# Kernel tuning notes

Measured on AMD Instinct MI355X. Metric: run time of the kernel, lower is better.

The kernel has to match this reference:

```python
import jax, jax.numpy as jnp
import numpy as np

D_M = 1024
NUM_TOK = 4096


def setup_inputs() -> dict:
    key = jax.random.key(0)
    ks = jax.random.split(key, 7)
    mk = lambda k, shp: jax.random.normal(k, shp, dtype=jnp.float32) * 0.02
    return {
        "X": jax.random.normal(ks[0], (D_M, NUM_TOK), dtype=jnp.float32),
        "W_Q": mk(ks[1], (D_M, D_M)),
        "W_K": mk(ks[2], (D_M, D_M)),
        "W_V": mk(ks[3], (D_M, D_M)),
        "W_O": mk(ks[4], (D_M, D_M)),
        "mlp_in": mk(ks[5], (D_M, D_M)),
        "mlp_out": mk(ks[6], (D_M, D_M)),
    }


def reference(X, W_Q, W_K, W_V, W_O, mlp_in, mlp_out):
    # X: [d_m, num_tok]; module transposes to tokens-major [N, d]
    Xt = X.T  # [N, d]
    N = Xt.shape[0]
    Q = Xt @ W_Q  # [N, d]
    K = Xt @ W_K  # [N, d]
    scores = Q @ K.T  # [N, N] -- NOTE: no 1/sqrt(d) scaling, as in the original
    causal = jnp.tril(jnp.ones((N, N), dtype=bool))  # keep lower triangle incl. diag
    scores = jnp.where(causal, scores, -jnp.inf)
    A = jax.nn.softmax(scores, axis=-1)  # [N, N]
    # original applies W_V then W_O to X BEFORE the attention mix
    RH = (Xt @ W_V) @ W_O  # [N, d]
    Xt = Xt + A @ RH  # residual + attention
    h = jax.nn.relu(Xt @ mlp_in)  # [N, d] (hidden dim == d_m in original)
    Xt = Xt + h @ mlp_out  # residual + MLP
    return Xt.T  # back to [d_m, num_tok]
```

## Files before the change

kernel.cpp:

```cpp
#include <hip/hip_runtime.h>
#include <stdint.h>
#include <stddef.h>

using f16 = _Float16;
typedef __attribute__((ext_vector_type(8))) _Float16 f16x8;
typedef __attribute__((ext_vector_type(4))) float f32x4;

__device__ __forceinline__ void async_copy16(const f16* g, f16* l) {
    __builtin_amdgcn_global_load_lds(
        (const __attribute__((address_space(1))) void*)g,
        (__attribute__((address_space(3))) void*)l, 16, 0, 0);
}

__global__ __launch_bounds__(256)
void prep_all(const float* __restrict__ X, float* __restrict__ Xtf,
              f16* __restrict__ Xth,
              const float* __restrict__ w0, const float* __restrict__ w1,
              const float* __restrict__ w2, const float* __restrict__ w3,
              const float* __restrict__ w4, const float* __restrict__ w5,
              f16* o0, f16* o1, f16* o2, f16* o3, f16* o4, f16* o5,
              int D, int NT) {
    __shared__ float tile[32][33];
    const int tx = threadIdx.x & 31, ty = threadIdx.x >> 5;
    int b = blockIdx.x;
    if (b < 4096) {
        const int c0 = (b & 127) * 32, r0 = (b >> 7) * 32;
#pragma unroll
        for (int j = 0; j < 4; j++)
            tile[ty + j * 8][tx] = X[(size_t)(r0 + ty + j * 8) * NT + c0 + tx];
        __syncthreads();
#pragma unroll
        for (int j = 0; j < 4; j++) {
            float v = tile[tx][ty + j * 8];
            size_t idx = (size_t)(c0 + ty + j * 8) * D + r0 + tx;
            Xtf[idx] = v;
            Xth[idx] = (f16)v;
        }
        return;
    }
    b -= 4096;
    const int z = b >> 10, r = b & 1023;
    const float* in = z == 0 ? w0 : z == 1 ? w1 : z == 2 ? w2 : z == 3 ? w3 : z == 4 ? w4 : w5;
    f16* out = z == 0 ? o0 : z == 1 ? o1 : z == 2 ? o2 : z == 3 ? o3 : z == 4 ? o4 : o5;
    const int c0 = (r & 31) * 32, r0 = (r >> 5) * 32;
    if (z < 3) {
#pragma unroll
        for (int j = 0; j < 4; j++) {
            size_t idx = (size_t)(r0 + ty + j * 8) * D + c0 + tx;
            out[idx] = (f16)in[idx];
        }
    } else {
#pragma unroll
        for (int j = 0; j < 4; j++)
            tile[ty + j * 8][tx] = in[(size_t)(r0 + ty + j * 8) * D + c0 + tx];
        __syncthreads();
#pragma unroll
        for (int j = 0; j < 4; j++)
            out[(size_t)(c0 + ty + j * 8) * D + r0 + tx] = (f16)tile[tx][ty + j * 8];
    }
}

__global__ __launch_bounds__(256)
void softmax_rows(f16* __restrict__ A, int N) {
    const int row = blockIdx.x, len = row + 1;
    const int lim = ((row >> 7) + 1) << 7;
    f16* a = A + (size_t)row * N;
    __shared__ float red[256];
    const int t = threadIdx.x;

    float v[16];
    float mx = -1e30f;
#pragma unroll
    for (int j = 0; j < 2; j++) {
        const int c = (t + j * 256) * 8;
        if (c < len) {
            f16x8 x = *(const f16x8*)(a + c);
#pragma unroll
            for (int e = 0; e < 8; e++) {
                float f = (c + e < len) ? (float)x[e] : -1e30f;
                v[j * 8 + e] = f;
                mx = fmaxf(mx, f);
            }
        } else {
#pragma unroll
            for (int e = 0; e < 8; e++) v[j * 8 + e] = -1e30f;
        }
    }
    red[t] = mx; __syncthreads();
    for (int o = 128; o > 0; o >>= 1) { if (t < o) red[t] = fmaxf(red[t], red[t + o]); __syncthreads(); }
    mx = red[0]; __syncthreads();

    float sum = 0.f;
#pragma unroll
    for (int k = 0; k < 16; k++) {
        float e = (v[k] > -1e29f) ? __expf(v[k] - mx) : 0.0f;
        v[k] = e;
        sum += e;
    }
    red[t] = sum; __syncthreads();
    for (int o = 128; o > 0; o >>= 1) { if (t < o) red[t] += red[t + o]; __syncthreads(); }
    const float inv = 1.0f / red[0];
#pragma unroll
    for (int j = 0; j < 2; j++) {
        const int c = (t + j * 256) * 8;
        if (c < lim) {
            f16x8 o8;
#pragma unroll
            for (int e = 0; e < 8; e++) o8[e] = (f16)(v[j * 8 + e] * inv);
            *(f16x8*)(a + c) = o8;
        }
    }
}

template <int MODE>
__device__ __forceinline__ void body64(
    f16* lA, f16* lB, const f16* __restrict__ A, const f16* __restrict__ B,
    f16* __restrict__ Ch, int m0, int n0, int N, int K, int lda, int Keff) {
    const int t = threadIdx.x;
    const int lane = t & 63, wave = t >> 6;
    const int wm = (wave >> 1) * 32, wn = (wave & 1) * 32;
    const int lm = lane & 15, lq = lane >> 4;
    const int sr = t >> 2, sc = (t & 3) * 8;

    f32x4 acc[2][2] = {};

    for (int k0 = 0; k0 < Keff; k0 += 128) {
#pragma unroll
        for (int r = 0; r < 4; r++)
            async_copy16(A + (size_t)(m0 + sr) * lda + k0 + r * 32 + sc,
                         lA + r * 2048 + t * 8);
#pragma unroll
        for (int r = 0; r < 4; r++)
            async_copy16(B + (size_t)(n0 + sr) * K + k0 + r * 32 + sc,
                         lB + r * 2048 + t * 8);
        __syncthreads();

#pragma unroll
        for (int kk = 0; kk < 4; kk++) {
            f16x8 af[2], bf[2];
#pragma unroll
            for (int i = 0; i < 2; i++)
                af[i] = *(const f16x8*)&lA[kk * 2048 + (wm + i * 16 + lm) * 32 + lq * 8];
#pragma unroll
            for (int j = 0; j < 2; j++)
                bf[j] = *(const f16x8*)&lB[kk * 2048 + (wn + j * 16 + lm) * 32 + lq * 8];
#pragma unroll
            for (int i = 0; i < 2; i++)
#pragma unroll
                for (int j = 0; j < 2; j++)
                    acc[i][j] = __builtin_amdgcn_mfma_f32_16x16x32_f16(
                        af[i], bf[j], acc[i][j], 0, 0, 0);
        }
        __syncthreads();
    }

#pragma unroll
    for (int i = 0; i < 2; i++) {
        const int row = m0 + wm + i * 16 + lq * 4;
#pragma unroll
        for (int j = 0; j < 2; j++) {
            const int col = n0 + wn + j * 16 + lm;
            f32x4 v = acc[i][j];
#pragma unroll
            for (int r = 0; r < 4; r++)
                Ch[(size_t)(row + r) * N + col] = (f16)v[r];
        }
    }
}

template <int BN, int MODE>
__device__ __forceinline__ void body128(
    f16* lA, f16* lB, const f16* __restrict__ A, const f16* __restrict__ B,
    float* __restrict__ Cf, f16* __restrict__ Ch, const float* __restrict__ resid,
    int m0, int n0, int M, int N, int K, int lda, int Keff) {
    const int t = threadIdx.x;
    const int lane = t & 63, wave = t >> 6;
    constexpr int WN = BN / 2;
    constexpr int NJ = WN / 16;
    const int wm = (wave >> 1) * 64, wn = (wave & 1) * WN;
    const int lm = lane & 15, lq = lane >> 4;
    const int srow = t >> 2, scol = (t & 3) * 8;

    f32x4 acc[4][NJ] = {};

    for (int k0 = 0; k0 < Keff; k0 += 64) {
#pragma unroll
        for (int r = 0; r < 4; r++) {
            const int row = (r & 1) * 64 + srow, kk = r >> 1;
            async_copy16(A + (size_t)(m0 + row) * lda + k0 + kk * 32 + scol,
                         lA + kk * 4096 + row * 32 + scol);
        }
        if constexpr (BN == 128) {
#pragma unroll
            for (int r = 0; r < 4; r++) {
                const int row = (r & 1) * 64 + srow, kk = r >> 1;
                async_copy16(B + (size_t)(n0 + row) * K + k0 + kk * 32 + scol,
                             lB + kk * 4096 + row * 32 + scol);
            }
        } else {
#pragma unroll
            for (int r = 0; r < 2; r++)
                async_copy16(B + (size_t)(n0 + srow) * K + k0 + r * 32 + scol,
                             lB + r * 2048 + srow * 32 + scol);
        }
        __syncthreads();

#pragma unroll
        for (int kk = 0; kk < 2; kk++) {
            f16x8 af[4], bf[NJ];
#pragma unroll
            for (int i = 0; i < 4; i++)
                af[i] = *(const f16x8*)&lA[kk * 4096 + (wm + i * 16 + lm) * 32 + lq * 8];
#pragma unroll
            for (int j = 0; j < NJ; j++)
                bf[j] = *(const f16x8*)&lB[kk * (BN * 32) + (wn + j * 16 + lm) * 32 + lq * 8];
#pragma unroll
            for (int i = 0; i < 4; i++)
#pragma unroll
                for (int j = 0; j < NJ; j++)
                    acc[i][j] = __builtin_amdgcn_mfma_f32_16x16x32_f16(
                        af[i], bf[j], acc[i][j], 0, 0, 0);
        }
        __syncthreads();
    }

#pragma unroll
    for (int i = 0; i < 4; i++) {
        const int row = m0 + wm + i * 16 + lq * 4;
#pragma unroll
        for (int j = 0; j < NJ; j++) {
            const int col = n0 + wn + j * 16 + lm;
            f32x4 v = acc[i][j];
#pragma unroll
            for (int r = 0; r < 4; r++) {
                if (MODE == 0) {
                    Ch[(size_t)(row + r) * N + col] = (f16)v[r];
                } else if (MODE == 2) {
                    float o = v[r] + resid[(size_t)(row + r) * N + col];
                    Cf[(size_t)(row + r) * N + col] = o;
                    Ch[(size_t)(row + r) * N + col] = (f16)o;
                } else if (MODE == 3) {
                    Ch[(size_t)(row + r) * N + col] = (f16)fmaxf(v[r], 0.0f);
                } else {
                    float o = v[r] + resid[(size_t)(row + r) * N + col];
                    Cf[(size_t)col * M + (row + r)] = o;
                }
            }
        }
    }
}

__global__ __launch_bounds__(256, 4)
void tiny_pair(const f16* Wkh, const f16* Wqh, f16* GT,
               const f16* Wot, const f16* Wvh, f16* HT) {
    __shared__ alignas(16) f16 smem[16384];
    const int b = blockIdx.x;
    if (b < 256)
        body64<0>(smem, smem + 8192, Wkh, Wqh, GT,
                  (b >> 4) * 64, (b & 15) * 64, 1024, 1024, 1024, 1024);
    else {
        const int r = b - 256;
        body64<0>(smem, smem + 8192, Wot, Wvh, HT,
                  (r >> 4) * 64, (r & 15) * 64, 1024, 1024, 1024, 1024);
    }
}

__global__ __launch_bounds__(256, 2)
void mid_pair(const f16* Xth, const f16* GT, f16* Qp,
              const f16* HT, f16* RHt) {
    __shared__ alignas(16) f16 smem[16384];
    const int x = blockIdx.x & 7;
    int s = blockIdx.x >> 3;
    if (s < 32) {
        const int m = x + 8 * (s >> 3), n = s & 7;
        body128<128, 0>(smem, smem + 8192, Xth, GT, nullptr, Qp, nullptr,
                        m * 128, n * 128, 4096, 1024, 1024, 1024, 1024);
    } else {
        s -= 32;
        const int n = x + 8 * (s >> 3), m = s & 7;
        body128<128, 0>(smem, smem + 8192, HT, Xth, nullptr, RHt, nullptr,
                        m * 128, n * 128, 1024, 4096, 1024, 1024, 1024);
    }
}

__global__ __launch_bounds__(256, 2)
void scores_tri(const f16* Qp, const f16* Xth, f16* Af) {
    __shared__ alignas(16) f16 smem[16384];
    const int x = blockIdx.x & 7;
    int s = blockIdx.x >> 3;
    int m = 0, n = 0;
#pragma unroll
    for (int q = 3; q >= 0; q--) {
        const int mm = 8 * q + ((q & 1) ? 7 - x : x);
        if (s < mm + 1) { m = mm; n = s; break; }
        s -= mm + 1;
    }
    body128<128, 0>(smem, smem + 8192, Qp, Xth, nullptr, Af, nullptr,
                    m * 128, n * 128, 4096, 4096, 1024, 1024, 1024);
}

template <int MODE, bool CAUSAL_K>
__global__ __launch_bounds__(256, 2)
void gemm_n64(const f16* __restrict__ A, const f16* __restrict__ B,
              float* __restrict__ Cf, f16* __restrict__ Ch,
              const float* __restrict__ resid, int M, int N, int K, int lda) {
    __shared__ alignas(16) f16 smem[12288];
    const int x = blockIdx.x & 7, s = blockIdx.x >> 3;
    const int qs = s >> 4, n = s & 15;
    int m;
    if (CAUSAL_K) {
        const int q = (qs == 0) ? 3 : (qs == 1) ? 2 : (qs == 2) ? 0 : 1;
        m = 8 * q + ((q & 1) ? 7 - x : x);
    } else {
        m = x + 8 * qs;
    }
    const int m0 = m * 128, n0 = n * 64;
    int Keff = K;
    if (CAUSAL_K) {
        Keff = m0 + 128;
        if (Keff > K) Keff = K;
    }
    body128<64, MODE>(smem, smem + 8192, A, B, Cf, Ch, resid,
                      m0, n0, M, N, K, lda, Keff);
}

extern "C" void kernel_launch(void* const* d_in, const int* in_sizes, int n_in,
                              void* d_out, int out_size, void* d_ws, size_t ws_size,
                              hipStream_t stream) {
    const int D = 1024, NT = 4096;
    const float* X = (const float*)d_in[0];
    const float* W[6] = {(const float*)d_in[1], (const float*)d_in[2],
                         (const float*)d_in[3], (const float*)d_in[4],
                         (const float*)d_in[5], (const float*)d_in[6]};
    char* ws = (char*)d_ws;
    auto MB = [](size_t x) { return x << 20; };

    float* Xtf  = (float*)(ws + MB(0));
    f16*   Xth  = (f16*)(ws + MB(16));
    f16*   Wqh  = (f16*)(ws + MB(24));
    f16*   Wkh  = (f16*)(ws + MB(26));
    f16*   Wvh  = (f16*)(ws + MB(28));
    f16*   Wot  = (f16*)(ws + MB(30));
    f16*   W4t  = (f16*)(ws + MB(32));
    f16*   W5t  = (f16*)(ws + MB(34));
    f16*   GT   = (f16*)(ws + MB(36));
    f16*   HT   = (f16*)(ws + MB(38));
    f16*   Qp   = (f16*)(ws + MB(40));
    f16*   Af   = (f16*)(ws + MB(48));
    f16*   RHt  = (f16*)(ws + MB(80));
    float* Y1f  = (float*)(ws + MB(88));
    f16*   Y1h  = (f16*)(ws + MB(104));
    f16*   hb   = (f16*)(ws + MB(40));
    float* outF = (float*)d_out;

    prep_all<<<10240, 256, 0, stream>>>(X, Xtf, Xth, W[0], W[1], W[2], W[3],
                                        W[4], W[5], Wqh, Wkh, Wvh, Wot, W4t,
                                        W5t, D, NT);

    tiny_pair<<<512, 256, 0, stream>>>(Wkh, Wqh, GT, Wot, Wvh, HT);

    mid_pair<<<512, 256, 0, stream>>>(Xth, GT, Qp, HT, RHt);

    scores_tri<<<528, 256, 0, stream>>>(Qp, Xth, Af);

    softmax_rows<<<NT, 256, 0, stream>>>(Af, NT);

    gemm_n64<2, true><<<512, 256, 0, stream>>>(
        Af, RHt, Y1f, Y1h, Xtf, NT, D, NT, NT);

    gemm_n64<3, false><<<512, 256, 0, stream>>>(
        Y1h, W4t, nullptr, hb, nullptr, NT, D, D, D);

    gemm_n64<4, false><<<512, 256, 0, stream>>>(
        hb, W5t, outF, nullptr, Y1f, NT, D, D, D);
}
```

Baseline: 259.5 us.

## Double-buffer LDS tiles and XOR-swizzle layout in GEMM bodies

Rewrites the shared GEMM bodies so the next K-tile is staged into a second LDS buffer with async global-to-LDS copies while MFMAs run on the current one, leaving one barrier per iteration instead of two. It also XOR-swizzles the 16-byte column chunks on both write and read to cut LDS bank conflicts. LDS per block doubles, and tiny_pair's occupancy hint drops from 4 to 2. The lone trailing barrier may not wait for the async loads to land before they are read, so correctness depends on how the compiler places its waits.

```diff
diff --git a/kernel.cpp b/kernel.cpp
--- a/kernel.cpp
+++ b/kernel.cpp
@@ -112,38 +112,45 @@
     }
 }
 
-template <int MODE>
-__device__ __forceinline__ void body64(
-    f16* lA, f16* lB, const f16* __restrict__ A, const f16* __restrict__ B,
-    f16* __restrict__ Ch, int m0, int n0, int N, int K, int lda, int Keff) {
+
+__device__ __forceinline__ void body64db(
+    f16* lds, const f16* __restrict__ A, const f16* __restrict__ B,
+    f16* __restrict__ Ch, int m0, int n0, int N, int K, int lda) {
     const int t = threadIdx.x;
     const int lane = t & 63, wave = t >> 6;
     const int wm = (wave >> 1) * 32, wn = (wave & 1) * 32;
     const int lm = lane & 15, lq = lane >> 4;
-    const int sr = t >> 2, sc = (t & 3) * 8;
+    const int srow = t >> 2;
+    const int gs = ((t & 3) ^ ((srow >> 1) & 3)) * 8;
+    const int rs = (lq ^ ((lm >> 1) & 3)) * 8;
+
+    auto stage = [&](f16* buf, int k0) {
+#pragma unroll
+        for (int r = 0; r < 4; r++)
+            async_copy16(A + (size_t)(m0 + srow) * lda + k0 + r * 32 + gs,
+                         buf + r * 2048 + t * 8);
+#pragma unroll
+        for (int r = 0; r < 4; r++)
+            async_copy16(B + (size_t)(n0 + srow) * K + k0 + r * 32 + gs,
+                         buf + 8192 + r * 2048 + t * 8);
+    };
 
     f32x4 acc[2][2] = {};
-
-    for (int k0 = 0; k0 < Keff; k0 += 128) {
-#pragma unroll
-        for (int r = 0; r < 4; r++)
-            async_copy16(A + (size_t)(m0 + sr) * lda + k0 + r * 32 + sc,
-                         lA + r * 2048 + t * 8);
-#pragma unroll
-        for (int r = 0; r < 4; r++)
-            async_copy16(B + (size_t)(n0 + sr) * K + k0 + r * 32 + sc,
-                         lB + r * 2048 + t * 8);
-        __syncthreads();
-
+    stage(lds, 0);
+    __syncthreads();
+    int cur = 0;
+    for (int k0 = 0; k0 < K; k0 += 128) {
+        f16* cb = lds + cur * 16384;
+        if (k0 + 128 < K) stage(lds + (cur ^ 1) * 16384, k0 + 128);
 #pragma unroll
         for (int kk = 0; kk < 4; kk++) {
             f16x8 af[2], bf[2];
 #pragma unroll
             for (int i = 0; i < 2; i++)
-                af[i] = *(const f16x8*)&lA[kk * 2048 + (wm + i * 16 + lm) * 32 + lq * 8];
+                af[i] = *(const f16x8*)&cb[kk * 2048 + (wm + i * 16 + lm) * 32 + rs];
 #pragma unroll
             for (int j = 0; j < 2; j++)
-                bf[j] = *(const f16x8*)&lB[kk * 2048 + (wn + j * 16 + lm) * 32 + lq * 8];
+                bf[j] = *(const f16x8*)&cb[8192 + kk * 2048 + (wn + j * 16 + lm) * 32 + rs];
 #pragma unroll
             for (int i = 0; i < 2; i++)
 #pragma unroll
@@ -152,6 +159,7 @@
                         af[i], bf[j], acc[i][j], 0, 0, 0);
         }
         __syncthreads();
+        cur ^= 1;
     }
 
 #pragma unroll
@@ -169,51 +177,57 @@
 }
 
 template <int BN, int MODE>
-__device__ __forceinline__ void body128(
-    f16* lA, f16* lB, const f16* __restrict__ A, const f16* __restrict__ B,
+__device__ __forceinline__ void body128db(
+    f16* lds, const f16* __restrict__ A, const f16* __restrict__ B,
     float* __restrict__ Cf, f16* __restrict__ Ch, const float* __restrict__ resid,
     int m0, int n0, int M, int N, int K, int lda, int Keff) {
     const int t = threadIdx.x;
     const int lane = t & 63, wave = t >> 6;
     constexpr int WN = BN / 2;
     constexpr int NJ = WN / 16;
+    constexpr int ASZ = 128 * 64;
+    constexpr int BSZ = BN * 64;
+    constexpr int BUF = ASZ + BSZ;
     const int wm = (wave >> 1) * 64, wn = (wave & 1) * WN;
     const int lm = lane & 15, lq = lane >> 4;
-    const int srow = t >> 2, scol = (t & 3) * 8;
+    const int srow = t >> 2;
+    const int gs = ((t & 3) ^ ((srow >> 1) & 3)) * 8;
+    const int rs = (lq ^ ((lm >> 1) & 3)) * 8;
+
+    auto stage = [&](f16* buf, int k0) {
+#pragma unroll
+        for (int r = 0; r < 4; r++)
+            async_copy16(A + (size_t)(m0 + (r & 1) * 64 + srow) * lda + k0 + (r >> 1) * 32 + gs,
+                         buf + r * 2048 + t * 8);
+        if constexpr (BN == 128) {
+#pragma unroll
+            for (int r = 0; r < 4; r++)
+                async_copy16(B + (size_t)(n0 + (r & 1) * 64 + srow) * K + k0 + (r >> 1) * 32 + gs,
+                             buf + ASZ + r * 2048 + t * 8);
+        } else {
+#pragma unroll
+            for (int r = 0; r < 2; r++)
+                async_copy16(B + (size_t)(n0 + srow) * K + k0 + r * 32 + gs,
+                             buf + ASZ + r * 2048 + t * 8);
+        }
+    };
 
     f32x4 acc[4][NJ] = {};
-
+    stage(lds, 0);
+    __syncthreads();
+    int cur = 0;
     for (int k0 = 0; k0 < Keff; k0 += 64) {
-#pragma unroll
-        for (int r = 0; r < 4; r++) {
-            const int row = (r & 1) * 64 + srow, kk = r >> 1;
-            async_copy16(A + (size_t)(m0 + row) * lda + k0 + kk * 32 + scol,
-                         lA + kk * 4096 + row * 32 + scol);
-        }
-        if constexpr (BN == 128) {
-#pragma unroll
-            for (int r = 0; r < 4; r++) {
-                const int row = (r & 1) * 64 + srow, kk = r >> 1;
-                async_copy16(B + (size_t)(n0 + row) * K + k0 + kk * 32 + scol,
-                             lB + kk * 4096 + row * 32 + scol);
-            }
-        } else {
-#pragma unroll
-            for (int r = 0; r < 2; r++)
-                async_copy16(B + (size_t)(n0 + srow) * K + k0 + r * 32 + scol,
-                             lB + r * 2048 + srow * 32 + scol);
-        }
-        __syncthreads();
-
+        f16* cb = lds + cur * BUF;
+        if (k0 + 64 < Keff) stage(lds + (cur ^ 1) * BUF, k0 + 64);
 #pragma unroll
         for (int kk = 0; kk < 2; kk++) {
             f16x8 af[4], bf[NJ];
 #pragma unroll
             for (int i = 0; i < 4; i++)
-                af[i] = *(const f16x8*)&lA[kk * 4096 + (wm + i * 16 + lm) * 32 + lq * 8];
+                af[i] = *(const f16x8*)&cb[kk * 4096 + (wm + i * 16 + lm) * 32 + rs];
 #pragma unroll
             for (int j = 0; j < NJ; j++)
-                bf[j] = *(const f16x8*)&lB[kk * (BN * 32) + (wn + j * 16 + lm) * 32 + lq * 8];
+                bf[j] = *(const f16x8*)&cb[ASZ + kk * (BN * 32) + (wn + j * 16 + lm) * 32 + rs];
 #pragma unroll
             for (int i = 0; i < 4; i++)
 #pragma unroll
@@ -222,6 +236,7 @@
                         af[i], bf[j], acc[i][j], 0, 0, 0);
         }
         __syncthreads();
+        cur ^= 1;
     }
 
 #pragma unroll
@@ -250,42 +265,42 @@
     }
 }
 
-__global__ __launch_bounds__(256, 4)
+__global__ __launch_bounds__(256, 2)
 void tiny_pair(const f16* Wkh, const f16* Wqh, f16* GT,
                const f16* Wot, const f16* Wvh, f16* HT) {
-    __shared__ alignas(16) f16 smem[16384];
+    __shared__ alignas(16) f16 smem[32768];
     const int b = blockIdx.x;
     if (b < 256)
-        body64<0>(smem, smem + 8192, Wkh, Wqh, GT,
-                  (b >> 4) * 64, (b & 15) * 64, 1024, 1024, 1024, 1024);
+        body64db(smem, Wkh, Wqh, GT,
+                 (b >> 4) * 64, (b & 15) * 64, 1024, 1024, 1024);
     else {
         const int r = b - 256;
-        body64<0>(smem, smem + 8192, Wot, Wvh, HT,
-                  (r >> 4) * 64, (r & 15) * 64, 1024, 1024, 1024, 1024);
+        body64db(smem, Wot, Wvh, HT,
+                 (r >> 4) * 64, (r & 15) * 64, 1024, 1024, 1024);
     }
 }
 
 __global__ __launch_bounds__(256, 2)
 void mid_pair(const f16* Xth, const f16* GT, f16* Qp,
               const f16* HT, f16* RHt) {
-    __shared__ alignas(16) f16 smem[16384];
+    __shared__ alignas(16) f16 smem[32768];
     const int x = blockIdx.x & 7;
     int s = blockIdx.x >> 3;
     if (s < 32) {
         const int m = x + 8 * (s >> 3), n = s & 7;
-        body128<128, 0>(smem, smem + 8192, Xth, GT, nullptr, Qp, nullptr,
-                        m * 128, n * 128, 4096, 1024, 1024, 1024, 1024);
+        body128db<128, 0>(smem, Xth, GT, nullptr, Qp, nullptr,
+                          m * 128, n * 128, 4096, 1024, 1024, 1024, 1024);
     } else {
         s -= 32;
         const int n = x + 8 * (s >> 3), m = s & 7;
-        body128<128, 0>(smem, smem + 8192, HT, Xth, nullptr, RHt, nullptr,
-                        m * 128, n * 128, 1024, 4096, 1024, 1024, 1024);
+        body128db<128, 0>(smem, HT, Xth, nullptr, RHt, nullptr,
+                          m * 128, n * 128, 1024, 4096, 1024, 1024, 1024);
     }
 }
 
 __global__ __launch_bounds__(256, 2)
 void scores_tri(const f16* Qp, const f16* Xth, f16* Af) {
-    __shared__ alignas(16) f16 smem[16384];
+    __shared__ alignas(16) f16 smem[32768];
     const int x = blockIdx.x & 7;
     int s = blockIdx.x >> 3;
     int m = 0, n = 0;
@@ -295,8 +310,8 @@
         if (s < mm + 1) { m = mm; n = s; break; }
         s -= mm + 1;
     }
-    body128<128, 0>(smem, smem + 8192, Qp, Xth, nullptr, Af, nullptr,
-                    m * 128, n * 128, 4096, 4096, 1024, 1024, 1024);
+    body128db<128, 0>(smem, Qp, Xth, nullptr, Af, nullptr,
+                      m * 128, n * 128, 4096, 4096, 1024, 1024, 1024);
 }
 
 template <int MODE, bool CAUSAL_K>
@@ -304,7 +319,7 @@
 void gemm_n64(const f16* __restrict__ A, const f16* __restrict__ B,
               float* __restrict__ Cf, f16* __restrict__ Ch,
               const float* __restrict__ resid, int M, int N, int K, int lda) {
-    __shared__ alignas(16) f16 smem[12288];
+    __shared__ alignas(16) f16 smem[24576];
     const int x = blockIdx.x & 7, s = blockIdx.x >> 3;
     const int qs = s >> 4, n = s & 15;
     int m;
@@ -320,8 +335,8 @@
         Keff = m0 + 128;
         if (Keff > K) Keff = K;
     }
-    body128<64, MODE>(smem, smem + 8192, A, B, Cf, Ch, resid,
-                      m0, n0, M, N, K, lda, Keff);
+    body128db<64, MODE>(smem, A, B, Cf, Ch, resid,
+                        m0, n0, M, N, K, lda, Keff);
 }
 
 extern "C" void kernel_launch(void* const* d_in, const int* in_sizes, int n_in,
```

Result: faster. 241.3 us (-7.0%).
